# Kernel optimization log

Measured on AMD Instinct MI355X. Metric: run time of the kernel, lower is better.

The kernel has to match this reference:

```python
import jax, jax.numpy as jnp
import numpy as np

TAU = 2.0      # LIF membrane time constant
VTH = 1.0      # firing threshold
ALPHA = 4.0    # sigmoid surrogate sharpness (spikingjelly default)
EPS = 1e-5     # BatchNorm eps


@jax.custom_vjp
def spike(x):
    # Heaviside forward, sigmoid surrogate backward
    return (x >= 0.0).astype(x.dtype)

def _spike_fwd(x):
    return (x >= 0.0).astype(x.dtype), x

def _spike_bwd(x, g):
    s = jax.nn.sigmoid(ALPHA * x)
    return (g * ALPHA * s * (1.0 - s),)

spike.defvjp(_spike_fwd, _spike_bwd)


def setup_inputs() -> dict:
    key = jax.random.key(0)
    k1, k2 = jax.random.split(key)
    T, B, C_in, C_out, M = 8, 16, 256, 256, 1024
    x = jax.random.normal(k1, (T, B, C_in, M), dtype=jnp.float32)
    W = jax.random.normal(k2, (C_out, C_in), dtype=jnp.float32) * 0.05  # 1x1 conv weight
    gamma = jnp.ones((C_out,), dtype=jnp.float32)
    beta = jnp.zeros((C_out,), dtype=jnp.float32)
    return {"x": x, "W": W, "gamma": gamma, "beta": beta}


def reference(x, W, gamma, beta):
    # 1x1 Conv1d over flattened (T*B) batch == channel contraction
    y = jnp.einsum('oc,tbcm->tbom', W, x)  # [T,B,C_out,M]
    # BatchNorm1d (training forward): per-channel stats over (T*B, M)
    mean = y.mean(axis=(0, 1, 3), keepdims=True)
    var = y.var(axis=(0, 1, 3), keepdims=True)
    y = (y - mean) * jax.lax.rsqrt(var + EPS)
    y = y * gamma[None, None, :, None] + beta[None, None, :, None]

    # Multi-step LIF: v <- v + (x - v)/tau; fire; hard reset to 0 (detached)
    def step(v, xt):
        v = v + (xt - v) / TAU
        s = spike(v - VTH)
        v = v * (1.0 - jax.lax.stop_gradient(s))
        return v, s

    v0 = jnp.zeros_like(y[0])
    _, spikes = jax.lax.scan(step, v0, y)
    return spikes  # [T,B,C_out,M]
```

## Files before the change

kernel.cpp:

```cpp
#include <hip/hip_runtime.h>

#define TT 8
#define BB 16
#define CC 256
#define MM 1024
#define NY 33554432


__global__ __launch_bounds__(256) void einsum_store(
    const float* __restrict__ x, const float* __restrict__ W,
    float* __restrict__ y)
{
    __shared__ float wt[CC][16];
    const int tid = threadIdx.x;
    const int lin = blockIdx.x;
    const int xcd = lin & 7;
    const int j   = lin >> 3;
    const int og  = j & 15;
    const int tb  = xcd * 16 + (j >> 4);
    const int m0  = tid * 4;

#pragma unroll
    for (int i = 0; i < 16; ++i)
        wt[tid][i] = W[(size_t)(og * 16 + i) * CC + tid];
    __syncthreads();

    const float* xs = x + (size_t)tb * (CC * MM) + m0;

    float a[16][4];
#pragma unroll
    for (int i = 0; i < 16; ++i)
#pragma unroll
        for (int q = 0; q < 4; ++q) a[i][q] = 0.0f;

    float4 xb[4];
#pragma unroll
    for (int q = 0; q < 4; ++q)
        xb[q] = *(const float4*)(xs + (size_t)q * MM);

    for (int cb = 0; cb < CC; cb += 4) {
        float4 xn[4];
        const bool more = (cb + 4 < CC);
        if (more) {
#pragma unroll
            for (int q = 0; q < 4; ++q)
                xn[q] = *(const float4*)(xs + (size_t)(cb + 4 + q) * MM);
        }
#pragma unroll
        for (int q = 0; q < 4; ++q) {
            const int c = cb + q;
            const float4 w0 = *(const float4*)&wt[c][0];
            const float4 w1 = *(const float4*)&wt[c][4];
            const float4 w2 = *(const float4*)&wt[c][8];
            const float4 w3 = *(const float4*)&wt[c][12];
            const float wv[16] = {w0.x, w0.y, w0.z, w0.w,
                                  w1.x, w1.y, w1.z, w1.w,
                                  w2.x, w2.y, w2.z, w2.w,
                                  w3.x, w3.y, w3.z, w3.w};
#pragma unroll
            for (int i = 0; i < 16; ++i) {
                a[i][0] = __fadd_rn(a[i][0], __fmul_rn(wv[i], xb[q].x));
                a[i][1] = __fadd_rn(a[i][1], __fmul_rn(wv[i], xb[q].y));
                a[i][2] = __fadd_rn(a[i][2], __fmul_rn(wv[i], xb[q].z));
                a[i][3] = __fadd_rn(a[i][3], __fmul_rn(wv[i], xb[q].w));
            }
        }
        if (more) {
#pragma unroll
            for (int q = 0; q < 4; ++q) xb[q] = xn[q];
        }
    }

#pragma unroll
    for (int i = 0; i < 16; ++i) {
        const int o = og * 16 + i;
        *(float4*)(y + ((size_t)tb * CC + o) * MM + m0) =
            make_float4(a[i][0], a[i][1], a[i][2], a[i][3]);
    }
}

__global__ __launch_bounds__(256) void mean_partial_y(
    const float* __restrict__ y, float* __restrict__ part)
{
    __shared__ float yrow[4][1024];
    __shared__ float scratch[4][64];
    const int tid  = threadIdx.x;
    const int g    = tid >> 6;
    const int lane = tid & 63;
    const size_t row = (size_t)blockIdx.x * 4 + g;
    const float* yr = y + row * MM;

#pragma unroll
    for (int q = 0; q < 4; ++q)
        *(float4*)&yrow[g][q * 256 + lane * 4] =
            *(const float4*)(yr + q * 256 + lane * 4);
    __syncthreads();

    {
        const int blk = lane >> 3;
        const int k   = lane & 7;
        const float* p = &yrow[g][blk * 128 + k];
        float r = p[0];
#pragma unroll
        for (int i = 1; i < 16; ++i) r = __fadd_rn(r, p[8 * i]);
        scratch[g][lane] = r;
    }
    __syncthreads();

    if (lane == 0) {
        float B[8];
#pragma unroll
        for (int b2 = 0; b2 < 8; ++b2) {
            const float* r = &scratch[g][b2 * 8];
            const float s01 = __fadd_rn(r[0], r[1]);
            const float s23 = __fadd_rn(r[2], r[3]);
            const float s45 = __fadd_rn(r[4], r[5]);
            const float s67 = __fadd_rn(r[6], r[7]);
            B[b2] = __fadd_rn(__fadd_rn(s01, s23), __fadd_rn(s45, s67));
        }
        const float c0 = __fadd_rn(B[0], B[1]);
        const float c1 = __fadd_rn(B[2], B[3]);
        const float c2 = __fadd_rn(B[4], B[5]);
        const float c3 = __fadd_rn(B[6], B[7]);
        part[row] = __fadd_rn(__fadd_rn(c0, c1), __fadd_rn(c2, c3));
    }
}

__global__ void reduce_mean(const float* __restrict__ part,
                            float* __restrict__ mv)
{
    const int o = threadIdx.x;
    float S = 0.0f;
    for (int tb = 0; tb < 128; ++tb)
        S = __fadd_rn(S, part[(size_t)tb * 256 + o]);
    mv[o] = S * (1.0f / 131072.0f);
}

__global__ __launch_bounds__(256) void var_partial_y(
    const float* __restrict__ y, const float* __restrict__ mv,
    float* __restrict__ part)
{
    __shared__ float yrow[4][1024];
    __shared__ float scratch[4][64];
    const int tid  = threadIdx.x;
    const int g    = tid >> 6;
    const int lane = tid & 63;
    const size_t row = (size_t)blockIdx.x * 4 + g;
    const float* yr = y + row * MM;
    const float mean = mv[row & 255];

#pragma unroll
    for (int q = 0; q < 4; ++q) {
        const float4 yv = *(const float4*)(yr + q * 256 + lane * 4);
        const float d0 = __fsub_rn(yv.x, mean);
        const float d1 = __fsub_rn(yv.y, mean);
        const float d2 = __fsub_rn(yv.z, mean);
        const float d3 = __fsub_rn(yv.w, mean);
        *(float4*)&yrow[g][q * 256 + lane * 4] =
            make_float4(__fmul_rn(d0, d0), __fmul_rn(d1, d1),
                        __fmul_rn(d2, d2), __fmul_rn(d3, d3));
    }
    __syncthreads();

    {
        const int blk = lane >> 3;
        const int k   = lane & 7;
        const float* p = &yrow[g][blk * 128 + k];
        float r = p[0];
#pragma unroll
        for (int i = 1; i < 16; ++i) r = __fadd_rn(r, p[8 * i]);
        scratch[g][lane] = r;
    }
    __syncthreads();

    if (lane == 0) {
        float B[8];
#pragma unroll
        for (int b2 = 0; b2 < 8; ++b2) {
            const float* r = &scratch[g][b2 * 8];
            const float s01 = __fadd_rn(r[0], r[1]);
            const float s23 = __fadd_rn(r[2], r[3]);
            const float s45 = __fadd_rn(r[4], r[5]);
            const float s67 = __fadd_rn(r[6], r[7]);
            B[b2] = __fadd_rn(__fadd_rn(s01, s23), __fadd_rn(s45, s67));
        }
        const float c0 = __fadd_rn(B[0], B[1]);
        const float c1 = __fadd_rn(B[2], B[3]);
        const float c2 = __fadd_rn(B[4], B[5]);
        const float c3 = __fadd_rn(B[6], B[7]);
        part[row] = __fadd_rn(__fadd_rn(c0, c1), __fadd_rn(c2, c3));
    }
}

__global__ void reduce_var(const float* __restrict__ part,
                           float* __restrict__ mv)
{
    const int o = threadIdx.x;
    float S = 0.0f;
    for (int tb = 0; tb < 128; ++tb)
        S = __fadd_rn(S, part[(size_t)tb * 256 + o]);
    const float var = S * (1.0f / 131072.0f);
    const float vp  = __fadd_rn(var, 1e-5f);
    mv[256 + o] = __fdiv_rn(1.0f, __fsqrt_rn(vp));
}

__global__ __launch_bounds__(256) void lif_from_y(
    const float* __restrict__ y, const float* __restrict__ mv,
    const float* __restrict__ gamma, const float* __restrict__ beta,
    float* __restrict__ out)
{
    const int tid = threadIdx.x;
    const int o = blockIdx.x;
    const int b = blockIdx.y;
    const int m0 = tid * 4;

    const float mean = mv[o];
    const float rs   = mv[256 + o];
    const float g    = gamma[o];
    const float be   = beta[o];

    float v0 = 0.0f, v1 = 0.0f, v2 = 0.0f, v3 = 0.0f;

    for (int t = 0; t < TT; ++t) {
        const size_t off = ((size_t)(t * BB + b) * CC + o) * MM + m0;
        const float4 yv = *(const float4*)(y + off);

        const float n0 = __fadd_rn(__fmul_rn(__fmul_rn(__fsub_rn(yv.x, mean), rs), g), be);
        const float n1 = __fadd_rn(__fmul_rn(__fmul_rn(__fsub_rn(yv.y, mean), rs), g), be);
        const float n2 = __fadd_rn(__fmul_rn(__fmul_rn(__fsub_rn(yv.z, mean), rs), g), be);
        const float n3 = __fadd_rn(__fmul_rn(__fmul_rn(__fsub_rn(yv.w, mean), rs), g), be);

        v0 = __fadd_rn(v0, __fmul_rn(__fsub_rn(n0, v0), 0.5f));
        v1 = __fadd_rn(v1, __fmul_rn(__fsub_rn(n1, v1), 0.5f));
        v2 = __fadd_rn(v2, __fmul_rn(__fsub_rn(n2, v2), 0.5f));
        v3 = __fadd_rn(v3, __fmul_rn(__fsub_rn(n3, v3), 0.5f));

        const bool s0 = (v0 >= 1.0f);
        const bool s1 = (v1 >= 1.0f);
        const bool s2 = (v2 >= 1.0f);
        const bool s3 = (v3 >= 1.0f);
        if (s0) v0 = 0.0f;
        if (s1) v1 = 0.0f;
        if (s2) v2 = 0.0f;
        if (s3) v3 = 0.0f;

        *(float4*)(out + off) = make_float4(s0 ? 1.0f : 0.0f, s1 ? 1.0f : 0.0f,
                                            s2 ? 1.0f : 0.0f, s3 ? 1.0f : 0.0f);
    }
}

__device__ __forceinline__ void e1_row4(
    const float* __restrict__ x, const float* __restrict__ W,
    int t, int b, int o, int m0,
    float& y0, float& y1, float& y2, float& y3)
{
    const float* xs = x + ((size_t)(t * BB + b) * CC) * MM + m0;
    const float* wr = W + (size_t)o * CC;
    y0 = 0.0f; y1 = 0.0f; y2 = 0.0f; y3 = 0.0f;
    for (int c = 0; c < CC; ++c) {
        const float wc = wr[c];
        const float4 xv = *(const float4*)(xs + (size_t)c * MM);
        y0 = __fadd_rn(y0, __fmul_rn(wc, xv.x));
        y1 = __fadd_rn(y1, __fmul_rn(wc, xv.y));
        y2 = __fadd_rn(y2, __fmul_rn(wc, xv.z));
        y3 = __fadd_rn(y3, __fmul_rn(wc, xv.w));
    }
}

__device__ __forceinline__ float np_pairwise_1024(
    const float* __restrict__ yrow, float* __restrict__ scratch, int tid)
{
    if (tid < 64) {
        const int blk = tid >> 3;
        const int k   = tid & 7;
        const float* p = yrow + blk * 128 + k;
        float r = p[0];
#pragma unroll
        for (int i = 1; i < 16; ++i) r = __fadd_rn(r, p[8 * i]);
        scratch[tid] = r;
    }
    __syncthreads();
    if (tid == 0) {
        float B[8];
#pragma unroll
        for (int blk = 0; blk < 8; ++blk) {
            const float* r = scratch + blk * 8;
            const float s01 = __fadd_rn(r[0], r[1]);
            const float s23 = __fadd_rn(r[2], r[3]);
            const float s45 = __fadd_rn(r[4], r[5]);
            const float s67 = __fadd_rn(r[6], r[7]);
            B[blk] = __fadd_rn(__fadd_rn(s01, s23), __fadd_rn(s45, s67));
        }
        const float c0 = __fadd_rn(B[0], B[1]);
        const float c1 = __fadd_rn(B[2], B[3]);
        const float c2 = __fadd_rn(B[4], B[5]);
        const float c3 = __fadd_rn(B[6], B[7]);
        scratch[64] = __fadd_rn(__fadd_rn(c0, c1), __fadd_rn(c2, c3));
    }
    __syncthreads();
    return scratch[64];
}

__global__ __launch_bounds__(256) void pass_mean_fb(
    const float* __restrict__ x, const float* __restrict__ W,
    float* __restrict__ part)
{
    __shared__ float yrow[1024];
    __shared__ float scratch[65];
    const int tid = threadIdx.x;
    const int o  = blockIdx.x;
    const int tb = blockIdx.y;
    const int m0 = tid * 4;
    float y0, y1, y2, y3;
    e1_row4(x, W, tb >> 4, tb & 15, o, m0, y0, y1, y2, y3);
    *(float4*)&yrow[m0] = make_float4(y0, y1, y2, y3);
    __syncthreads();
    const float P = np_pairwise_1024(yrow, scratch, tid);
    if (tid == 0) part[(size_t)tb * 256 + o] = P;
}

__global__ __launch_bounds__(256) void pass_var_fb(
    const float* __restrict__ x, const float* __restrict__ W,
    const float* __restrict__ mv, float* __restrict__ part)
{
    __shared__ float yrow[1024];
    __shared__ float scratch[65];
    const int tid = threadIdx.x;
    const int o  = blockIdx.x;
    const int tb = blockIdx.y;
    const int m0 = tid * 4;
    const float mean = mv[o];
    float y0, y1, y2, y3;
    e1_row4(x, W, tb >> 4, tb & 15, o, m0, y0, y1, y2, y3);
    const float d0 = __fsub_rn(y0, mean);
    const float d1 = __fsub_rn(y1, mean);
    const float d2 = __fsub_rn(y2, mean);
    const float d3 = __fsub_rn(y3, mean);
    *(float4*)&yrow[m0] = make_float4(__fmul_rn(d0, d0), __fmul_rn(d1, d1),
                                      __fmul_rn(d2, d2), __fmul_rn(d3, d3));
    __syncthreads();
    const float P = np_pairwise_1024(yrow, scratch, tid);
    if (tid == 0) part[(size_t)tb * 256 + o] = P;
}

__global__ __launch_bounds__(256) void pass_lif_fb(
    const float* __restrict__ x, const float* __restrict__ W,
    const float* __restrict__ mv,
    const float* __restrict__ gamma, const float* __restrict__ beta,
    float* __restrict__ out)
{
    const int tid = threadIdx.x;
    const int o = blockIdx.x;
    const int b = blockIdx.y;
    const int m0 = tid * 4;
    const float mean = mv[o];
    const float rs   = mv[256 + o];
    const float g    = gamma[o];
    const float be   = beta[o];
    float v0 = 0.0f, v1 = 0.0f, v2 = 0.0f, v3 = 0.0f;
    for (int t = 0; t < TT; ++t) {
        float y0, y1, y2, y3;
        e1_row4(x, W, t, b, o, m0, y0, y1, y2, y3);
        const float n0 = __fadd_rn(__fmul_rn(__fmul_rn(__fsub_rn(y0, mean), rs), g), be);
        const float n1 = __fadd_rn(__fmul_rn(__fmul_rn(__fsub_rn(y1, mean), rs), g), be);
        const float n2 = __fadd_rn(__fmul_rn(__fmul_rn(__fsub_rn(y2, mean), rs), g), be);
        const float n3 = __fadd_rn(__fmul_rn(__fmul_rn(__fsub_rn(y3, mean), rs), g), be);
        v0 = __fadd_rn(v0, __fmul_rn(__fsub_rn(n0, v0), 0.5f));
        v1 = __fadd_rn(v1, __fmul_rn(__fsub_rn(n1, v1), 0.5f));
        v2 = __fadd_rn(v2, __fmul_rn(__fsub_rn(n2, v2), 0.5f));
        v3 = __fadd_rn(v3, __fmul_rn(__fsub_rn(n3, v3), 0.5f));
        const bool s0 = (v0 >= 1.0f);
        const bool s1 = (v1 >= 1.0f);
        const bool s2 = (v2 >= 1.0f);
        const bool s3 = (v3 >= 1.0f);
        if (s0) v0 = 0.0f;
        if (s1) v1 = 0.0f;
        if (s2) v2 = 0.0f;
        if (s3) v3 = 0.0f;
        const size_t off = ((size_t)(t * BB + b) * CC + o) * MM + m0;
        *(float4*)(out + off) = make_float4(s0 ? 1.0f : 0.0f, s1 ? 1.0f : 0.0f,
                                            s2 ? 1.0f : 0.0f, s3 ? 1.0f : 0.0f);
    }
}

extern "C" void kernel_launch(void* const* d_in, const int* in_sizes, int n_in,
                              void* d_out, int out_size, void* d_ws, size_t ws_size,
                              hipStream_t stream)
{
    const float* x     = (const float*)d_in[0];
    const float* W     = (const float*)d_in[1];
    const float* gamma = (const float*)d_in[2];
    const float* beta  = (const float*)d_in[3];
    float* out = (float*)d_out;

    const size_t need = ((size_t)NY + 128 * 256 + 512) * sizeof(float);

    if (ws_size >= need) {
        float* y    = (float*)d_ws;
        float* part = y + NY;
        float* mv   = part + 128 * 256;

        einsum_store<<<dim3(2048), dim3(256), 0, stream>>>(x, W, y);
        mean_partial_y<<<dim3(8192), dim3(256), 0, stream>>>(y, part);
        reduce_mean<<<dim3(1), dim3(256), 0, stream>>>(part, mv);
        var_partial_y<<<dim3(8192), dim3(256), 0, stream>>>(y, mv, part);
        reduce_var<<<dim3(1), dim3(256), 0, stream>>>(part, mv);
        lif_from_y<<<dim3(256, 16), dim3(256), 0, stream>>>(y, mv, gamma, beta, out);
    } else {
        float* part = (float*)d_ws;
        float* mv   = part + 128 * 256;
        pass_mean_fb<<<dim3(256, 128), dim3(256), 0, stream>>>(x, W, part);
        reduce_mean<<<dim3(1), dim3(256), 0, stream>>>(part, mv);
        pass_var_fb<<<dim3(256, 128), dim3(256), 0, stream>>>(x, W, mv, part);
        reduce_var<<<dim3(1), dim3(256), 0, stream>>>(part, mv);
        pass_lif_fb<<<dim3(256, 16), dim3(256), 0, stream>>>(x, W, mv, gamma, beta, out);
    }
}
```

Measured before the change: 477.7 us.

## Fuse per-row mean partials into einsum epilogue and fold var reduce into LIF

The einsum kernel now computes each output row's partial sum from its register accumulators through padded shared memory. It writes the partial directly, so the separate mean_partial_y pass that re-read all of y from memory is gone. The reduce_var launch is also dropped: every LIF block recomputes the variance reduction over 128 partials for its channel. This removes one full read of the 128MB intermediate and one tiny launch, in exchange for extra syncs in the einsum epilogue and redundant per-block reduction work in the LIF kernel.

```diff
diff --git a/kernel.cpp b/kernel.cpp
--- a/kernel.cpp
+++ b/kernel.cpp
@@ -7,11 +7,13 @@
 #define NY 33554432
 
 
-__global__ __launch_bounds__(256) void einsum_store(
+__global__ __launch_bounds__(256) void einsum_store_mean(
     const float* __restrict__ x, const float* __restrict__ W,
-    float* __restrict__ y)
+    float* __restrict__ y, float* __restrict__ part)
 {
     __shared__ float wt[CC][16];
+    __shared__ float yrow[4][1056];
+    __shared__ float scratch[4][64];
     const int tid = threadIdx.x;
     const int lin = blockIdx.x;
     const int xcd = lin & 7;
@@ -77,52 +79,49 @@
         *(float4*)(y + ((size_t)tb * CC + o) * MM + m0) =
             make_float4(a[i][0], a[i][1], a[i][2], a[i][3]);
     }
-}
-
-__global__ __launch_bounds__(256) void mean_partial_y(
-    const float* __restrict__ y, float* __restrict__ part)
-{
-    __shared__ float yrow[4][1024];
-    __shared__ float scratch[4][64];
-    const int tid  = threadIdx.x;
+
     const int g    = tid >> 6;
     const int lane = tid & 63;
-    const size_t row = (size_t)blockIdx.x * 4 + g;
-    const float* yr = y + row * MM;
-
-#pragma unroll
-    for (int q = 0; q < 4; ++q)
-        *(float4*)&yrow[g][q * 256 + lane * 4] =
-            *(const float4*)(yr + q * 256 + lane * 4);
-    __syncthreads();
-
-    {
-        const int blk = lane >> 3;
-        const int k   = lane & 7;
-        const float* p = &yrow[g][blk * 128 + k];
-        float r = p[0];
-#pragma unroll
-        for (int i = 1; i < 16; ++i) r = __fadd_rn(r, p[8 * i]);
-        scratch[g][lane] = r;
-    }
-    __syncthreads();
-
-    if (lane == 0) {
-        float B[8];
-#pragma unroll
-        for (int b2 = 0; b2 < 8; ++b2) {
-            const float* r = &scratch[g][b2 * 8];
-            const float s01 = __fadd_rn(r[0], r[1]);
-            const float s23 = __fadd_rn(r[2], r[3]);
-            const float s45 = __fadd_rn(r[4], r[5]);
-            const float s67 = __fadd_rn(r[6], r[7]);
-            B[b2] = __fadd_rn(__fadd_rn(s01, s23), __fadd_rn(s45, s67));
-        }
-        const float c0 = __fadd_rn(B[0], B[1]);
-        const float c1 = __fadd_rn(B[2], B[3]);
-        const float c2 = __fadd_rn(B[4], B[5]);
-        const float c3 = __fadd_rn(B[6], B[7]);
-        part[row] = __fadd_rn(__fadd_rn(c0, c1), __fadd_rn(c2, c3));
+    const int blk  = m0 >> 7;
+    const int off  = m0 & 127;
+#pragma unroll
+    for (int r = 0; r < 4; ++r) {
+        __syncthreads();
+#pragma unroll
+        for (int g2 = 0; g2 < 4; ++g2) {
+            const int i = r * 4 + g2;
+            *(float4*)&yrow[g2][blk * 132 + off] =
+                make_float4(a[i][0], a[i][1], a[i][2], a[i][3]);
+        }
+        __syncthreads();
+        {
+            const int b2 = lane >> 3;
+            const int k  = lane & 7;
+            const float* p = &yrow[g][b2 * 132 + k];
+            float rr = p[0];
+#pragma unroll
+            for (int i2 = 1; i2 < 16; ++i2) rr = __fadd_rn(rr, p[8 * i2]);
+            scratch[g][lane] = rr;
+        }
+        __syncthreads();
+        if (lane == 0) {
+            float Bv[8];
+#pragma unroll
+            for (int b2 = 0; b2 < 8; ++b2) {
+                const float* rp = &scratch[g][b2 * 8];
+                const float s01 = __fadd_rn(rp[0], rp[1]);
+                const float s23 = __fadd_rn(rp[2], rp[3]);
+                const float s45 = __fadd_rn(rp[4], rp[5]);
+                const float s67 = __fadd_rn(rp[6], rp[7]);
+                Bv[b2] = __fadd_rn(__fadd_rn(s01, s23), __fadd_rn(s45, s67));
+            }
+            const float c0 = __fadd_rn(Bv[0], Bv[1]);
+            const float c1 = __fadd_rn(Bv[2], Bv[3]);
+            const float c2 = __fadd_rn(Bv[4], Bv[5]);
+            const float c3 = __fadd_rn(Bv[6], Bv[7]);
+            part[(size_t)tb * 256 + og * 16 + r * 4 + g] =
+                __fadd_rn(__fadd_rn(c0, c1), __fadd_rn(c2, c3));
+        }
     }
 }
 
@@ -192,30 +191,26 @@
     }
 }
 
-__global__ void reduce_var(const float* __restrict__ part,
-                           float* __restrict__ mv)
-{
-    const int o = threadIdx.x;
+__global__ __launch_bounds__(256) void lif_from_y(
+    const float* __restrict__ y, const float* __restrict__ mv,
+    const float* __restrict__ part,
+    const float* __restrict__ gamma, const float* __restrict__ beta,
+    float* __restrict__ out)
+{
+    const int tid = threadIdx.x;
+    const int o = blockIdx.x;
+    const int b = blockIdx.y;
+    const int m0 = tid * 4;
+
+    const float mean = mv[o];
+
     float S = 0.0f;
     for (int tb = 0; tb < 128; ++tb)
         S = __fadd_rn(S, part[(size_t)tb * 256 + o]);
     const float var = S * (1.0f / 131072.0f);
     const float vp  = __fadd_rn(var, 1e-5f);
-    mv[256 + o] = __fdiv_rn(1.0f, __fsqrt_rn(vp));
-}
-
-__global__ __launch_bounds__(256) void lif_from_y(
-    const float* __restrict__ y, const float* __restrict__ mv,
-    const float* __restrict__ gamma, const float* __restrict__ beta,
-    float* __restrict__ out)
-{
-    const int tid = threadIdx.x;
-    const int o = blockIdx.x;
-    const int b = blockIdx.y;
-    const int m0 = tid * 4;
-
-    const float mean = mv[o];
-    const float rs   = mv[256 + o];
+    const float rs  = __fdiv_rn(1.0f, __fsqrt_rn(vp));
+
     const float g    = gamma[o];
     const float be   = beta[o];
 
@@ -247,6 +242,18 @@
         *(float4*)(out + off) = make_float4(s0 ? 1.0f : 0.0f, s1 ? 1.0f : 0.0f,
                                             s2 ? 1.0f : 0.0f, s3 ? 1.0f : 0.0f);
     }
+}
+
+__global__ void reduce_var(const float* __restrict__ part,
+                           float* __restrict__ mv)
+{
+    const int o = threadIdx.x;
+    float S = 0.0f;
+    for (int tb = 0; tb < 128; ++tb)
+        S = __fadd_rn(S, part[(size_t)tb * 256 + o]);
+    const float var = S * (1.0f / 131072.0f);
+    const float vp  = __fadd_rn(var, 1e-5f);
+    mv[256 + o] = __fdiv_rn(1.0f, __fsqrt_rn(vp));
 }
 
 __device__ __forceinline__ void e1_row4(
@@ -400,12 +407,10 @@
         float* part = y + NY;
         float* mv   = part + 128 * 256;
 
-        einsum_store<<<dim3(2048), dim3(256), 0, stream>>>(x, W, y);
-        mean_partial_y<<<dim3(8192), dim3(256), 0, stream>>>(y, part);
+        einsum_store_mean<<<dim3(2048), dim3(256), 0, stream>>>(x, W, y, part);
         reduce_mean<<<dim3(1), dim3(256), 0, stream>>>(part, mv);
         var_partial_y<<<dim3(8192), dim3(256), 0, stream>>>(y, mv, part);
-        reduce_var<<<dim3(1), dim3(256), 0, stream>>>(part, mv);
-        lif_from_y<<<dim3(256, 16), dim3(256), 0, stream>>>(y, mv, gamma, beta, out);
+        lif_from_y<<<dim3(256, 16), dim3(256), 0, stream>>>(y, mv, part, gamma, beta, out);
     } else {
         float* part = (float*)d_ws;
         float* mv   = part + 128 * 256;
```

After: 469.5 us. About the same (-1.7%).
